# Kernel tuning notes

Hardware: AMD Instinct MI355X
Metric: run time of the kernel (lower is better)

The kernel has to match this reference:

```python
import jax, jax.numpy as jnp
import numpy as np

TAU = 1.0
EXP_ORDER = 12
LN_ORDER = 16
CLAMP = 5.0
LN_EPS = 1e-30


def _exp_taylor(x, order):
    # Horner evaluation of sum_{k=0}^{order} x^k / k!
    r = jnp.ones_like(x)
    for k in range(order, 0, -1):
        r = 1.0 + x * r / k
    return r


def _ln_taylor(y, order):
    # Taylor series of ln(y) about 1: sum_{k=1}^{order} (-1)^{k+1} (y-1)^k / k (Horner)
    z = y - 1.0
    r = jnp.zeros_like(z)
    for k in range(order, 0, -1):
        r = 1.0 / k - z * r
    return z * r


def _eml(ex, ey):
    # eml(x, y) = exp(x) + ln(y), both via Taylor series ('taylor' backend).
    return _exp_taylor(ex, EXP_ORDER) + _ln_taylor(ey, LN_ORDER)


def _gumbel_softmax(key, logits_bt, tau):
    g = jax.random.gumbel(key, logits_bt.shape, dtype=logits_bt.dtype)
    return jax.nn.softmax((logits_bt + g) / tau, axis=-1)


def _forward(x, logits_list, key):
    B, n_vars = x.shape
    x_exp = x[:, None, :]  # [B, 1, V]
    prev = None
    for level, logits in enumerate(logits_list):
        T, n_nodes, n_choices, _ = logits.shape
        key, kL, kR = jax.random.split(key, 3)
        lb = jnp.broadcast_to(logits[None, ..., 0], (B, T, n_nodes, n_choices))
        rb = jnp.broadcast_to(logits[None, ..., 1], (B, T, n_nodes, n_choices))
        left_w = _gumbel_softmax(kL, lb, TAU)   # [B,T,nodes,choices]
        right_w = _gumbel_softmax(kR, rb, TAU)
        shape = (B, T, n_nodes)
        cands = [jnp.ones(shape, x.dtype)]
        for v in range(n_vars):
            cands.append(jnp.broadcast_to(x_exp[:, :, v:v + 1], shape))
        cl = list(cands)
        cr = list(cands)
        if level > 0:
            cl.append(prev[:, :, 0::2])
            cr.append(prev[:, :, 1::2])
        eml_x = jnp.sum(jnp.stack(cl, axis=-1) * left_w, axis=-1)
        eml_y = jnp.sum(jnp.stack(cr, axis=-1) * right_w, axis=-1)
        eml_x = jnp.clip(eml_x, -CLAMP, CLAMP)
        eml_y = jnp.clip(eml_y, LN_EPS, None)
        prev = _eml(eml_x, eml_y)  # [B, T, n_nodes]
    return prev[..., 0]  # [B, T]


def setup_inputs() -> dict:
    key = jax.random.key(0)
    ks = jax.random.split(key, 7)
    B, T, n_vars, depth = 2048, 128, 4, 6
    nodes = [2 ** (depth - 1 - l) for l in range(depth)]
    inp = {"x": jax.random.normal(ks[0], (B, n_vars), dtype=jnp.float32)}
    for l in range(depth):
        n_choices = 1 + n_vars + (0 if l == 0 else 1)
        inp[f"logits_l{l}"] = 0.1 * jax.random.normal(
            ks[l + 1], (T, nodes[l], n_choices, 2), dtype=jnp.float32)
    return inp


def reference(x, logits_l0, logits_l1, logits_l2, logits_l3, logits_l4, logits_l5):
    logits_list = [logits_l0, logits_l1, logits_l2, logits_l3, logits_l4, logits_l5]
    return _forward(x, logits_list, jax.random.key(42))
```

## Files before the change

kernel.cpp:

```cpp
#include <hip/hip_runtime.h>
#include <stdint.h>

#define BLOCK 128

struct KeySet {
  uint32_t k0L[6], k1L[6], k2L[6], k0R[6], k1R[6], k2R[6];
};

__host__ inline void tf2x32(uint32_t k0, uint32_t k1, uint32_t x0, uint32_t x1,
                            uint32_t& o0, uint32_t& o1) {
  const uint32_t k2 = k0 ^ k1 ^ 0x1BD11BDAu;
  x0 += k0; x1 += k1;
#define TFR(r) { x0 += x1; x1 = (x1 << (r)) | (x1 >> (32 - (r))); x1 ^= x0; }
  TFR(13) TFR(15) TFR(26) TFR(6)
  x0 += k1; x1 += k2 + 1u;
  TFR(17) TFR(29) TFR(16) TFR(24)
  x0 += k2; x1 += k0 + 2u;
  TFR(13) TFR(15) TFR(26) TFR(6)
  x0 += k0; x1 += k1 + 3u;
  TFR(17) TFR(29) TFR(16) TFR(24)
  x0 += k1; x1 += k2 + 4u;
  TFR(13) TFR(15) TFR(26) TFR(6)
  x0 += k2; x1 += k0 + 5u;
#undef TFR
  o0 = x0; o1 = x1;
}

__device__ __forceinline__ float wgt(uint32_t bits) {
  const float tiny = 1.17549435e-38f;
  float f = __uint_as_float((bits >> 9) | 0x3f800000u) - 1.0f;
  float u = fmaxf(f, tiny);
  float v = __builtin_amdgcn_logf(u);
  return __builtin_amdgcn_rcpf(-v);
}

__device__ __forceinline__ float expT(float x) {
  float r = 2.0876756987868099e-9f;
  r = fmaf(r, x, 2.5052108385441719e-8f);
  r = fmaf(r, x, 2.7557319223985893e-7f);
  r = fmaf(r, x, 2.7557319223985888e-6f);
  r = fmaf(r, x, 2.4801587301587302e-5f);
  r = fmaf(r, x, 1.9841269841269841e-4f);
  r = fmaf(r, x, 1.3888888888888889e-3f);
  r = fmaf(r, x, 8.3333333333333332e-3f);
  r = fmaf(r, x, 4.1666666666666664e-2f);
  r = fmaf(r, x, 1.6666666666666666e-1f);
  r = fmaf(r, x, 0.5f);
  r = fmaf(r, x, 1.0f);
  r = fmaf(r, x, 1.0f);
  return r;
}

__device__ __forceinline__ float lnT(float y) {
  const float inv[15] = {1.0f/15.0f, 1.0f/14.0f, 1.0f/13.0f, 1.0f/12.0f,
                         1.0f/11.0f, 0.1f, 1.0f/9.0f, 0.125f, 1.0f/7.0f, 1.0f/6.0f,
                         0.2f, 0.25f, 1.0f/3.0f, 0.5f, 1.0f};
  float z = y - 1.0f;
  float r = 1.0f/16.0f;
#pragma unroll
  for (int i = 0; i < 15; ++i) r = fmaf(-z, r, inv[i]);
  return z * r;
}

template<int C, bool HP>
__device__ __forceinline__ float node_eval(
    const float* __restrict__ w8,
    const uint32_t K0[2], const uint32_t K1[2], const uint32_t K2[2],
    uint32_t xL, uint32_t xR,
    float4 xv, float pl, float pr) {
  constexpr int N = 2 * C;
  uint32_t a0[N], a1[N];
#pragma unroll
  for (int i = 0; i < N; ++i) {
    const int s = (i < C) ? 0 : 1;
    a0[i] = K0[s];
    a1[i] = ((i < C) ? xL : xR) + (uint32_t)(i < C ? i : i - C);
  }
#define HALF(r) \
  _Pragma("unroll") for (int i = 0; i < N; ++i) { \
    a0[i] += a1[i]; \
    a1[i] = __builtin_rotateleft32(a1[i], (r)); \
    a1[i] ^= a0[i]; }
#define INJ(A, B, add) \
  _Pragma("unroll") for (int i = 0; i < N; ++i) { \
    const int s = (i < C) ? 0 : 1; \
    a0[i] += A[s]; a1[i] += B[s] + (add); }
  HALF(13) HALF(15) HALF(26) HALF(6)
  INJ(K1, K2, 1u)
  HALF(17) HALF(29) HALF(16) HALF(24)
  INJ(K2, K0, 2u)
  HALF(13) HALF(15) HALF(26) HALF(6)
  INJ(K0, K1, 3u)
  HALF(17) HALF(29) HALF(16) HALF(24)
  INJ(K1, K2, 4u)
  HALF(13) HALF(15) HALF(26) HALF(6)
#undef HALF
#undef INJ
  float wv[N];
#pragma unroll
  for (int i = 0; i < N; ++i) {
    const int s = (i < C) ? 0 : 1;
    wv[i] = wgt((a0[i] + K2[s]) ^ (a1[i] + K0[s] + 5u));
  }
  float e = w8[0] * wv[0];
  float denL = e, numL = e;
  e = w8[1] * wv[1]; denL += e; numL = fmaf(e, xv.x, numL);
  e = w8[2] * wv[2]; denL += e; numL = fmaf(e, xv.y, numL);
  e = w8[3] * wv[3]; denL += e; numL = fmaf(e, xv.z, numL);
  e = w8[4] * wv[4]; denL += e; numL = fmaf(e, xv.w, numL);
  if constexpr (C == 6) { e = w8[5] * wv[5]; denL += e; numL = fmaf(e, pl, numL); }
  e = w8[8] * wv[C];
  float denR = e, numR = e;
  e = w8[9]  * wv[C + 1]; denR += e; numR = fmaf(e, xv.x, numR);
  e = w8[10] * wv[C + 2]; denR += e; numR = fmaf(e, xv.y, numR);
  e = w8[11] * wv[C + 3]; denR += e; numR = fmaf(e, xv.z, numR);
  e = w8[12] * wv[C + 4]; denR += e; numR = fmaf(e, xv.w, numR);
  if constexpr (C == 6) { e = w8[13] * wv[N - 1]; denR += e; numR = fmaf(e, pr, numR); }
  float ex = numL * __builtin_amdgcn_rcpf(denL);
  float ey = numR * __builtin_amdgcn_rcpf(denR);
  ex = __builtin_amdgcn_fmed3f(ex, -5.0f, 5.0f);
  ey = fmaxf(ey, 1e-30f);
  return expT(ex) + lnT(ey);
}

template<int C, bool HP>
__device__ __forceinline__ void level_run(int nodes, const float* __restrict__ wl,
    const uint32_t* __restrict__ kk,
    uint32_t bt, uint32_t stride, float4 xv, float* __restrict__ pv) {
  const uint32_t K0[2] = {kk[0], kk[3]};
  const uint32_t K1[2] = {kk[1], kk[4]};
  const uint32_t K2[2] = {kk[2], kk[5]};
  const uint32_t xbL = bt * stride + kk[1];
  const uint32_t xbR = bt * stride + kk[4];
  for (int n = 0; n < nodes; ++n) {
    float pl = 0.0f, pr = 0.0f;
    if constexpr (HP) {
      pl = pv[(2 * n) * BLOCK];
      pr = pv[(2 * n + 1) * BLOCK];
    }
    float r = node_eval<C, HP>(wl + n * 16, K0, K1, K2,
                               xbL + (uint32_t)(n * C), xbR + (uint32_t)(n * C),
                               xv, pl, pr);
    pv[n * BLOCK] = r;
  }
}

template<int C>
__device__ __forceinline__ void stage(const float* __restrict__ g, float* __restrict__ ws,
                                      int t, int N, int woff, int tid) {
  const int total = N * C * 2;
  const float* src = g + t * total;
  for (int i = tid; i < total; i += BLOCK) {
    int n = i / (2 * C);
    int rem = i - n * 2 * C;
    int c = rem >> 1, s = rem & 1;
    ws[woff + n * 16 + s * 8 + c] =
        __builtin_amdgcn_exp2f(fmaf(src[i], 1.4426950408889634f, -24.0f));
  }
}

__global__ __launch_bounds__(BLOCK, 4) void eml_kernel(
    const float* __restrict__ x,
    const float* __restrict__ g0, const float* __restrict__ g1,
    const float* __restrict__ g2, const float* __restrict__ g3,
    const float* __restrict__ g4, const float* __restrict__ g5,
    float* __restrict__ out, KeySet ks) {
  __shared__ float wz[1008];
  __shared__ float pvs[32 * BLOCK];
  const int tid = threadIdx.x;
  const int t = blockIdx.x & 127;
  const int chunk = blockIdx.x >> 7;

  stage<5>(g0, wz, t, 32,   0, tid);
  stage<6>(g1, wz, t, 16, 512, tid);
  stage<6>(g2, wz, t,  8, 768, tid);
  stage<6>(g3, wz, t,  4, 896, tid);
  stage<6>(g4, wz, t,  2, 960, tid);
  stage<6>(g5, wz, t,  1, 992, tid);
  __syncthreads();

  const int b = chunk * BLOCK + tid;
  const uint32_t bt = (uint32_t)(b * 128 + t);
  const float4 xv = reinterpret_cast<const float4*>(x)[b];
  float* pv = &pvs[tid];

  uint32_t kk[6][6];
#pragma unroll
  for (int l = 0; l < 6; ++l) {
    kk[l][0] = ks.k0L[l]; kk[l][1] = ks.k1L[l]; kk[l][2] = ks.k2L[l];
    kk[l][3] = ks.k0R[l]; kk[l][4] = ks.k1R[l]; kk[l][5] = ks.k2R[l];
  }

  level_run<5, false>(32, wz,       kk[0], bt, 160u, xv, pv);
  level_run<6, true >(16, wz + 512, kk[1], bt,  96u, xv, pv);
  level_run<6, true >( 8, wz + 768, kk[2], bt,  48u, xv, pv);
  level_run<6, true >( 4, wz + 896, kk[3], bt,  24u, xv, pv);
  level_run<6, true >( 2, wz + 960, kk[4], bt,  12u, xv, pv);
  level_run<6, true >( 1, wz + 992, kk[5], bt,   6u, xv, pv);

  out[bt] = pvs[tid];
}

extern "C" void kernel_launch(void* const* d_in, const int* in_sizes, int n_in,
                              void* d_out, int out_size, void* d_ws, size_t ws_size,
                              hipStream_t stream) {
  const float* x  = (const float*)d_in[0];
  const float* g0 = (const float*)d_in[1];
  const float* g1 = (const float*)d_in[2];
  const float* g2 = (const float*)d_in[3];
  const float* g3 = (const float*)d_in[4];
  const float* g4 = (const float*)d_in[5];
  const float* g5 = (const float*)d_in[6];
  float* out = (float*)d_out;

  KeySet ks;
  uint32_t K0 = 0u, K1 = 42u;
  for (int l = 0; l < 6; ++l) {
    uint32_t n0, n1, a0, a1, c0, c1;
    tf2x32(K0, K1, 0u, 0u, n0, n1);
    tf2x32(K0, K1, 0u, 1u, a0, a1);
    tf2x32(K0, K1, 0u, 2u, c0, c1);
    ks.k0L[l] = a0; ks.k1L[l] = a1; ks.k2L[l] = a0 ^ a1 ^ 0x1BD11BDAu;
    ks.k0R[l] = c0; ks.k1R[l] = c1; ks.k2R[l] = c0 ^ c1 ^ 0x1BD11BDAu;
    K0 = n0; K1 = n1;
  }

  eml_kernel<<<dim3(2048), dim3(BLOCK), 0, stream>>>(x, g0, g1, g2, g3, g4, g5, out, ks);
}
```

Before: 351.9 us.

## Fuse tree levels pairwise to keep intermediates in registers

Restructures the level-by-level tree evaluation so two levels are computed together per loop iteration: pairs of child nodes are evaluated into registers and immediately combined into their parent. This halves the shared-memory scratch (16 instead of 32 rows per thread) and removes many LDS stores and loads of intermediate node values. The cost is larger unrolled loop bodies, which may raise register pressure and code size.

```diff
diff --git a/kernel.cpp b/kernel.cpp
--- a/kernel.cpp
+++ b/kernel.cpp
@@ -123,28 +123,6 @@
   return expT(ex) + lnT(ey);
 }
 
-template<int C, bool HP>
-__device__ __forceinline__ void level_run(int nodes, const float* __restrict__ wl,
-    const uint32_t* __restrict__ kk,
-    uint32_t bt, uint32_t stride, float4 xv, float* __restrict__ pv) {
-  const uint32_t K0[2] = {kk[0], kk[3]};
-  const uint32_t K1[2] = {kk[1], kk[4]};
-  const uint32_t K2[2] = {kk[2], kk[5]};
-  const uint32_t xbL = bt * stride + kk[1];
-  const uint32_t xbR = bt * stride + kk[4];
-  for (int n = 0; n < nodes; ++n) {
-    float pl = 0.0f, pr = 0.0f;
-    if constexpr (HP) {
-      pl = pv[(2 * n) * BLOCK];
-      pr = pv[(2 * n + 1) * BLOCK];
-    }
-    float r = node_eval<C, HP>(wl + n * 16, K0, K1, K2,
-                               xbL + (uint32_t)(n * C), xbR + (uint32_t)(n * C),
-                               xv, pl, pr);
-    pv[n * BLOCK] = r;
-  }
-}
-
 template<int C>
 __device__ __forceinline__ void stage(const float* __restrict__ g, float* __restrict__ ws,
                                       int t, int N, int woff, int tid) {
@@ -159,6 +137,20 @@
   }
 }
 
+struct LvlKeys {
+  uint32_t K0[2], K1[2], K2[2];
+  uint32_t xL, xR;
+};
+
+__device__ __forceinline__ LvlKeys mk(const uint32_t* kk, uint32_t bt, uint32_t stride) {
+  LvlKeys r;
+  r.K0[0] = kk[0]; r.K1[0] = kk[1]; r.K2[0] = kk[2];
+  r.K0[1] = kk[3]; r.K1[1] = kk[4]; r.K2[1] = kk[5];
+  r.xL = bt * stride + kk[1];
+  r.xR = bt * stride + kk[4];
+  return r;
+}
+
 __global__ __launch_bounds__(BLOCK, 4) void eml_kernel(
     const float* __restrict__ x,
     const float* __restrict__ g0, const float* __restrict__ g1,
@@ -166,7 +158,7 @@
     const float* __restrict__ g4, const float* __restrict__ g5,
     float* __restrict__ out, KeySet ks) {
   __shared__ float wz[1008];
-  __shared__ float pvs[32 * BLOCK];
+  __shared__ float pvs[16 * BLOCK];
   const int tid = threadIdx.x;
   const int t = blockIdx.x & 127;
   const int chunk = blockIdx.x >> 7;
@@ -190,15 +182,44 @@
     kk[l][0] = ks.k0L[l]; kk[l][1] = ks.k1L[l]; kk[l][2] = ks.k2L[l];
     kk[l][3] = ks.k0R[l]; kk[l][4] = ks.k1R[l]; kk[l][5] = ks.k2R[l];
   }
-
-  level_run<5, false>(32, wz,       kk[0], bt, 160u, xv, pv);
-  level_run<6, true >(16, wz + 512, kk[1], bt,  96u, xv, pv);
-  level_run<6, true >( 8, wz + 768, kk[2], bt,  48u, xv, pv);
-  level_run<6, true >( 4, wz + 896, kk[3], bt,  24u, xv, pv);
-  level_run<6, true >( 2, wz + 960, kk[4], bt,  12u, xv, pv);
-  level_run<6, true >( 1, wz + 992, kk[5], bt,   6u, xv, pv);
-
-  out[bt] = pvs[tid];
+  const LvlKeys kA = mk(kk[0], bt, 160u);
+  const LvlKeys kB = mk(kk[1], bt,  96u);
+  const LvlKeys kC = mk(kk[2], bt,  48u);
+  const LvlKeys kD = mk(kk[3], bt,  24u);
+  const LvlKeys kE = mk(kk[4], bt,  12u);
+  const LvlKeys kF = mk(kk[5], bt,   6u);
+
+  for (int n = 0; n < 16; ++n) {
+    const uint32_t o = (uint32_t)(10 * n);
+    float pl = node_eval<5, false>(wz + (2 * n) * 16, kA.K0, kA.K1, kA.K2,
+                                   kA.xL + o, kA.xR + o, xv, 0.0f, 0.0f);
+    float pr = node_eval<5, false>(wz + (2 * n + 1) * 16, kA.K0, kA.K1, kA.K2,
+                                   kA.xL + o + 5u, kA.xR + o + 5u, xv, 0.0f, 0.0f);
+    pv[n * BLOCK] = node_eval<6, true>(wz + 512 + n * 16, kB.K0, kB.K1, kB.K2,
+                                       kB.xL + (uint32_t)(6 * n), kB.xR + (uint32_t)(6 * n),
+                                       xv, pl, pr);
+  }
+  for (int n = 0; n < 4; ++n) {
+    float qa = pv[(4 * n) * BLOCK], qb = pv[(4 * n + 1) * BLOCK];
+    float qc = pv[(4 * n + 2) * BLOCK], qd = pv[(4 * n + 3) * BLOCK];
+    const uint32_t o = (uint32_t)(12 * n);
+    float pl = node_eval<6, true>(wz + 768 + (2 * n) * 16, kC.K0, kC.K1, kC.K2,
+                                  kC.xL + o, kC.xR + o, xv, qa, qb);
+    float pr = node_eval<6, true>(wz + 768 + (2 * n + 1) * 16, kC.K0, kC.K1, kC.K2,
+                                  kC.xL + o + 6u, kC.xR + o + 6u, xv, qc, qd);
+    pv[n * BLOCK] = node_eval<6, true>(wz + 896 + n * 16, kD.K0, kD.K1, kD.K2,
+                                       kD.xL + (uint32_t)(6 * n), kD.xR + (uint32_t)(6 * n),
+                                       xv, pl, pr);
+  }
+  {
+    float qa = pv[0], qb = pv[BLOCK], qc = pv[2 * BLOCK], qd = pv[3 * BLOCK];
+    float pl = node_eval<6, true>(wz + 960, kE.K0, kE.K1, kE.K2,
+                                  kE.xL, kE.xR, xv, qa, qb);
+    float pr = node_eval<6, true>(wz + 960 + 16, kE.K0, kE.K1, kE.K2,
+                                  kE.xL + 6u, kE.xR + 6u, xv, qc, qd);
+    out[bt] = node_eval<6, true>(wz + 992, kF.K0, kF.K1, kF.K2,
+                                 kF.xL, kF.xR, xv, pl, pr);
+  }
 }
 
 extern "C" void kernel_launch(void* const* d_in, const int* in_sizes, int n_in,
```

New measurement: 354.1 us. About the same (+0.6%).

## Split each node's left/right operands across lane pairs and fuse levels pairwise

Applied to the files above, without the earlier changes.

Each batch element is now handled by two adjacent lanes: one computes the left (exp) operand's RNG and softmax and the other the right (ln) operand, combined via a shuffle. Levels are fused two at a time so intermediate results stay in registers, which cuts shared-memory traffic and shrinks the per-block scratch buffer. Block size doubles and launch bounds allow more blocks per CU. Both lanes still evaluate both polynomials and the per-lane selects add some redundant work.

```diff
diff --git a/kernel.cpp b/kernel.cpp
--- a/kernel.cpp
+++ b/kernel.cpp
@@ -1,7 +1,8 @@
 #include <hip/hip_runtime.h>
 #include <stdint.h>
 
-#define BLOCK 128
+#define BLOCK 256
+#define PAIRS 128
 
 struct KeySet {
   uint32_t k0L[6], k1L[6], k2L[6], k0R[6], k1R[6], k2R[6];
@@ -62,87 +63,52 @@
   return z * r;
 }
 
-template<int C, bool HP>
-__device__ __forceinline__ float node_eval(
-    const float* __restrict__ w8,
-    const uint32_t K0[2], const uint32_t K1[2], const uint32_t K2[2],
-    uint32_t xL, uint32_t xR,
-    float4 xv, float pl, float pr) {
-  constexpr int N = 2 * C;
-  uint32_t a0[N], a1[N];
-#pragma unroll
-  for (int i = 0; i < N; ++i) {
-    const int s = (i < C) ? 0 : 1;
-    a0[i] = K0[s];
-    a1[i] = ((i < C) ? xL : xR) + (uint32_t)(i < C ? i : i - C);
-  }
+template<int C>
+__device__ __forceinline__ float node_pair(
+    const float* __restrict__ w8p,
+    uint32_t k0, uint32_t k1, uint32_t k2,
+    uint32_t xb,
+    float4 xv, float pc, uint32_t p) {
+  uint32_t a0[C], a1[C];
+#pragma unroll
+  for (int i = 0; i < C; ++i) { a0[i] = k0; a1[i] = xb + (uint32_t)i; }
 #define HALF(r) \
-  _Pragma("unroll") for (int i = 0; i < N; ++i) { \
+  _Pragma("unroll") for (int i = 0; i < C; ++i) { \
     a0[i] += a1[i]; \
     a1[i] = __builtin_rotateleft32(a1[i], (r)); \
     a1[i] ^= a0[i]; }
 #define INJ(A, B, add) \
-  _Pragma("unroll") for (int i = 0; i < N; ++i) { \
-    const int s = (i < C) ? 0 : 1; \
-    a0[i] += A[s]; a1[i] += B[s] + (add); }
+  _Pragma("unroll") for (int i = 0; i < C; ++i) { a0[i] += (A); a1[i] += (B) + (add); }
   HALF(13) HALF(15) HALF(26) HALF(6)
-  INJ(K1, K2, 1u)
+  INJ(k1, k2, 1u)
   HALF(17) HALF(29) HALF(16) HALF(24)
-  INJ(K2, K0, 2u)
+  INJ(k2, k0, 2u)
   HALF(13) HALF(15) HALF(26) HALF(6)
-  INJ(K0, K1, 3u)
+  INJ(k0, k1, 3u)
   HALF(17) HALF(29) HALF(16) HALF(24)
-  INJ(K1, K2, 4u)
+  INJ(k1, k2, 4u)
   HALF(13) HALF(15) HALF(26) HALF(6)
 #undef HALF
 #undef INJ
-  float wv[N];
-#pragma unroll
-  for (int i = 0; i < N; ++i) {
-    const int s = (i < C) ? 0 : 1;
-    wv[i] = wgt((a0[i] + K2[s]) ^ (a1[i] + K0[s] + 5u));
-  }
-  float e = w8[0] * wv[0];
-  float denL = e, numL = e;
-  e = w8[1] * wv[1]; denL += e; numL = fmaf(e, xv.x, numL);
-  e = w8[2] * wv[2]; denL += e; numL = fmaf(e, xv.y, numL);
-  e = w8[3] * wv[3]; denL += e; numL = fmaf(e, xv.z, numL);
-  e = w8[4] * wv[4]; denL += e; numL = fmaf(e, xv.w, numL);
-  if constexpr (C == 6) { e = w8[5] * wv[5]; denL += e; numL = fmaf(e, pl, numL); }
-  e = w8[8] * wv[C];
-  float denR = e, numR = e;
-  e = w8[9]  * wv[C + 1]; denR += e; numR = fmaf(e, xv.x, numR);
-  e = w8[10] * wv[C + 2]; denR += e; numR = fmaf(e, xv.y, numR);
-  e = w8[11] * wv[C + 3]; denR += e; numR = fmaf(e, xv.z, numR);
-  e = w8[12] * wv[C + 4]; denR += e; numR = fmaf(e, xv.w, numR);
-  if constexpr (C == 6) { e = w8[13] * wv[N - 1]; denR += e; numR = fmaf(e, pr, numR); }
-  float ex = numL * __builtin_amdgcn_rcpf(denL);
-  float ey = numR * __builtin_amdgcn_rcpf(denR);
-  ex = __builtin_amdgcn_fmed3f(ex, -5.0f, 5.0f);
-  ey = fmaxf(ey, 1e-30f);
-  return expT(ex) + lnT(ey);
-}
-
-template<int C, bool HP>
-__device__ __forceinline__ void level_run(int nodes, const float* __restrict__ wl,
-    const uint32_t* __restrict__ kk,
-    uint32_t bt, uint32_t stride, float4 xv, float* __restrict__ pv) {
-  const uint32_t K0[2] = {kk[0], kk[3]};
-  const uint32_t K1[2] = {kk[1], kk[4]};
-  const uint32_t K2[2] = {kk[2], kk[5]};
-  const uint32_t xbL = bt * stride + kk[1];
-  const uint32_t xbR = bt * stride + kk[4];
-  for (int n = 0; n < nodes; ++n) {
-    float pl = 0.0f, pr = 0.0f;
-    if constexpr (HP) {
-      pl = pv[(2 * n) * BLOCK];
-      pr = pv[(2 * n + 1) * BLOCK];
-    }
-    float r = node_eval<C, HP>(wl + n * 16, K0, K1, K2,
-                               xbL + (uint32_t)(n * C), xbR + (uint32_t)(n * C),
-                               xv, pl, pr);
-    pv[n * BLOCK] = r;
-  }
+  float wv[C];
+#pragma unroll
+  for (int i = 0; i < C; ++i) wv[i] = wgt((a0[i] + k2) ^ (a1[i] + (k0 + 5u)));
+  float4 wa = *reinterpret_cast<const float4*>(w8p);
+  float e = wa.x * wv[0];
+  float den = e, num = e;
+  e = wa.y * wv[1]; den += e; num = fmaf(e, xv.x, num);
+  e = wa.z * wv[2]; den += e; num = fmaf(e, xv.y, num);
+  e = wa.w * wv[3]; den += e; num = fmaf(e, xv.z, num);
+  e = w8p[4] * wv[4]; den += e; num = fmaf(e, xv.w, num);
+  if constexpr (C == 6) { e = w8p[5] * wv[5]; den += e; num = fmaf(e, pc, num); }
+  float val = num * __builtin_amdgcn_rcpf(den);
+  float vx = __builtin_amdgcn_fmed3f(val, -5.0f, 5.0f);
+  float vy = fmaxf(val, 1e-30f);
+  float v = p ? vy : vx;
+  float pe = expT(v);
+  float pl = lnT(v);
+  float part = p ? pl : pe;
+  return part + __shfl_xor(part, 1);
 }
 
 template<int C>
@@ -159,14 +125,14 @@
   }
 }
 
-__global__ __launch_bounds__(BLOCK, 4) void eml_kernel(
+__global__ __launch_bounds__(BLOCK, 8) void eml_kernel(
     const float* __restrict__ x,
     const float* __restrict__ g0, const float* __restrict__ g1,
     const float* __restrict__ g2, const float* __restrict__ g3,
     const float* __restrict__ g4, const float* __restrict__ g5,
     float* __restrict__ out, KeySet ks) {
   __shared__ float wz[1008];
-  __shared__ float pvs[32 * BLOCK];
+  __shared__ float pvs[16 * PAIRS];
   const int tid = threadIdx.x;
   const int t = blockIdx.x & 127;
   const int chunk = blockIdx.x >> 7;
@@ -179,26 +145,60 @@
   stage<6>(g5, wz, t,  1, 992, tid);
   __syncthreads();
 
-  const int b = chunk * BLOCK + tid;
+  const int pair = tid >> 1;
+  const uint32_t p = (uint32_t)(tid & 1);
+  const int b = chunk * PAIRS + pair;
   const uint32_t bt = (uint32_t)(b * 128 + t);
   const float4 xv = reinterpret_cast<const float4*>(x)[b];
-  float* pv = &pvs[tid];
-
-  uint32_t kk[6][6];
+  float* pv = &pvs[pair];
+  const int p8 = (int)(p * 8u);
+
+  uint32_t K0[6], K1[6], K2[6], XB[6];
+  const uint32_t strides[6] = {160u, 96u, 48u, 24u, 12u, 6u};
 #pragma unroll
   for (int l = 0; l < 6; ++l) {
-    kk[l][0] = ks.k0L[l]; kk[l][1] = ks.k1L[l]; kk[l][2] = ks.k2L[l];
-    kk[l][3] = ks.k0R[l]; kk[l][4] = ks.k1R[l]; kk[l][5] = ks.k2R[l];
-  }
-
-  level_run<5, false>(32, wz,       kk[0], bt, 160u, xv, pv);
-  level_run<6, true >(16, wz + 512, kk[1], bt,  96u, xv, pv);
-  level_run<6, true >( 8, wz + 768, kk[2], bt,  48u, xv, pv);
-  level_run<6, true >( 4, wz + 896, kk[3], bt,  24u, xv, pv);
-  level_run<6, true >( 2, wz + 960, kk[4], bt,  12u, xv, pv);
-  level_run<6, true >( 1, wz + 992, kk[5], bt,   6u, xv, pv);
-
-  out[bt] = pvs[tid];
+    K0[l] = p ? ks.k0R[l] : ks.k0L[l];
+    K1[l] = p ? ks.k1R[l] : ks.k1L[l];
+    K2[l] = p ? ks.k2R[l] : ks.k2L[l];
+    XB[l] = bt * strides[l] + K1[l];
+  }
+
+  for (int n = 0; n < 16; ++n) {
+    const uint32_t o = (uint32_t)(10 * n);
+    float rl = node_pair<5>(wz + (2 * n) * 16 + p8, K0[0], K1[0], K2[0],
+                            XB[0] + o, xv, 0.0f, p);
+    float rr = node_pair<5>(wz + (2 * n + 1) * 16 + p8, K0[0], K1[0], K2[0],
+                            XB[0] + o + 5u, xv, 0.0f, p);
+    float pc = p ? rr : rl;
+    float rn = node_pair<6>(wz + 512 + n * 16 + p8, K0[1], K1[1], K2[1],
+                            XB[1] + (uint32_t)(6 * n), xv, pc, p);
+    if (!p) pv[n * PAIRS] = rn;
+  }
+  for (int n = 0; n < 4; ++n) {
+    const uint32_t o = (uint32_t)(12 * n);
+    float pcA = pv[(4 * n + (int)p) * PAIRS];
+    float pcB = pv[(4 * n + 2 + (int)p) * PAIRS];
+    float rl = node_pair<6>(wz + 768 + (2 * n) * 16 + p8, K0[2], K1[2], K2[2],
+                            XB[2] + o, xv, pcA, p);
+    float rr = node_pair<6>(wz + 768 + (2 * n + 1) * 16 + p8, K0[2], K1[2], K2[2],
+                            XB[2] + o + 6u, xv, pcB, p);
+    float pc = p ? rr : rl;
+    float rn = node_pair<6>(wz + 896 + n * 16 + p8, K0[3], K1[3], K2[3],
+                            XB[3] + (uint32_t)(6 * n), xv, pc, p);
+    if (!p) pv[n * PAIRS] = rn;
+  }
+  {
+    float pcA = pv[((int)p) * PAIRS];
+    float pcB = pv[(2 + (int)p) * PAIRS];
+    float rl = node_pair<6>(wz + 960 + p8, K0[4], K1[4], K2[4],
+                            XB[4], xv, pcA, p);
+    float rr = node_pair<6>(wz + 960 + 16 + p8, K0[4], K1[4], K2[4],
+                            XB[4] + 6u, xv, pcB, p);
+    float pc = p ? rr : rl;
+    float rf = node_pair<6>(wz + 992 + p8, K0[5], K1[5], K2[5],
+                            XB[5], xv, pc, p);
+    if (!p) out[bt] = rf;
+  }
 }
 
 extern "C" void kernel_launch(void* const* d_in, const int* in_sizes, int n_in,
```

Measured after the change: 354.9 us. No clear change (+0.8%).
